# Kernel tuning notes

Measured on AMD Instinct MI355X. Metric: run time of the kernel, lower is better.

Reference implementation:

```python
import jax, jax.numpy as jnp
import numpy as np
import math

N, E, D, H = 1536, 49152, 512, 8
DH = D // H  # head dim = 64
SCALE = 256.0 * math.sqrt(2.0)  # rel_dists scaling in forward


def sinusoidal_pe(x, d):
    """x: [...] float positions -> [..., d] interleaved sin/cos encoding."""
    div = jnp.exp(jnp.arange(0, d, 2, dtype=jnp.float32) * (-math.log(10000.0) / d))
    ang = x[..., None] * div  # [..., d//2]
    return jnp.stack([jnp.sin(ang), jnp.cos(ang)], axis=-1).reshape(*x.shape, d)


def setup_inputs() -> dict:
    key = jax.random.key(0)
    ks = jax.random.split(key, 8)
    features = jax.random.normal(ks[0], (N, D), dtype=jnp.float32)
    edge_index = jax.random.randint(ks[1], (2, E), 0, N, dtype=jnp.int64)
    edge_attr = jax.random.uniform(ks[2], (E,), dtype=jnp.float32)  # normalized distances
    pos = jax.random.uniform(ks[3], (N, 2), dtype=jnp.float32)  # unused by forward
    s = 1.0 / math.sqrt(D)  # ~xavier-uniform bound sqrt(6/(D+D))... use simple symmetric init
    Wq = jax.random.uniform(ks[4], (D, D), minval=-s, maxval=s, dtype=jnp.float32)
    Wk = jax.random.uniform(ks[5], (D, D), minval=-s, maxval=s, dtype=jnp.float32)
    Wv = jax.random.uniform(ks[6], (D, D), minval=-s, maxval=s, dtype=jnp.float32)
    bq = jnp.zeros((D,), jnp.float32)
    bk = jnp.zeros((D,), jnp.float32)
    bv = jnp.zeros((D,), jnp.float32)
    return dict(features=features, edge_index=edge_index, edge_attr=edge_attr, pos=pos,
                Wq=Wq, bq=bq, Wk=Wk, bk=bk, Wv=Wv, bv=bv)


def reference(features, edge_index, edge_attr, pos, Wq, bq, Wk, bk, Wv, bv):
    # batch dim is 1 in the original (features.unsqueeze(0)); we omit it.
    q = (features @ Wq.T + bq).reshape(N, H, DH).transpose(1, 0, 2)  # [H,N,DH]
    k = (features @ Wk.T + bk).reshape(N, H, DH).transpose(1, 0, 2)
    v = (features @ Wv.T + bv).reshape(N, H, DH).transpose(1, 0, 2)

    qk = jnp.einsum('hqd,hrd->hqr', q, k)  # [H,N,N]

    # to_dense_adj: scatter-add edge_attr into dense [N,N], then scale
    rel = jnp.zeros((N, N), jnp.float32).at[edge_index[0], edge_index[1]].add(edge_attr) * SCALE
    # embed_k and embed_q are identical parameter-free sinusoidal encodings of rel
    rk = sinusoidal_pe(rel, DH)  # [N,N,DH]

    # original: qk + q.rk + k.rq + (q_repeat*k_repeat == qk)  => 2*qk + q.rk + k.rk
    logits = 2.0 * qk \
        + jnp.einsum('hqd,qrd->hqr', q, rk) \
        + jnp.einsum('hrd,qrd->hqr', k, rk)
    attn = jax.nn.softmax(logits / math.sqrt(DH), axis=-1)  # [H,N,N]

    out = jnp.einsum('hqr,hrd->hqd', attn, v)  # [H,N,DH]
    out = out.transpose(1, 0, 2).reshape(N, D)  # [N,D]
    return out.max(axis=0)  # [D] max-pool over nodes (MIL pooling)
```

## Files before the change

kernel.cpp:

```cpp
#include <hip/hip_runtime.h>
#include <cmath>


constexpr int Nn  = 1536;
constexpr int Dd  = 512;
constexpr int Hh  = 8;
constexpr int DHd = 64;
constexpr int SPLITS = 8;
constexpr float SCALE_F = 362.03867196751236f;
constexpr float M0 = 8.0f;

typedef float f4 __attribute__((ext_vector_type(4)));
typedef int   i4 __attribute__((ext_vector_type(4)));
typedef __attribute__((ext_vector_type(4))) float f32x4;
typedef __attribute__((ext_vector_type(8))) short bf16x8;

__device__ inline unsigned short bf16_rne(float x) {
    unsigned u = __float_as_uint(x);
    unsigned r = u + 0x7fff + ((u >> 16) & 1);
    return (unsigned short)(r >> 16);
}
__device__ inline float bf16_tof(unsigned short h) {
    return __uint_as_float(((unsigned)h) << 16);
}

__global__ __launch_bounds__(256) void pack_fw_k(
    const float* __restrict__ feat,
    const float* __restrict__ Wq, const float* __restrict__ Wk, const float* __restrict__ Wv,
    unsigned short* __restrict__ pFh, unsigned short* __restrict__ pFl,
    unsigned short* __restrict__ pWh, unsigned short* __restrict__ pWl)
{
    int tg = blockIdx.x * 256 + threadIdx.x;
    int type = blockIdx.y;
    int L = tg & 63;
    int kc = (tg >> 6) & 15;
    int t10 = tg >> 10;
    const float* src;
    unsigned short *oh, *ol;
    int row, col;
    if (type == 0) {
        src = feat; oh = pFh; ol = pFl;
        row = t10 * 16 + (L & 15);
        col = kc * 32 + (L >> 4) * 8;
    } else {
        int z = t10 >> 5, nt = t10 & 31;
        src = (z == 0) ? Wq : (z == 1) ? Wk : Wv;
        oh = pWh; ol = pWl;
        row = nt * 16 + (L & 15);
        col = kc * 32 + (L >> 4) * 8;
    }
    f4 a = *(const f4*)(src + (size_t)row * Dd + col);
    f4 b = *(const f4*)(src + (size_t)row * Dd + col + 4);
    float x[8];
    #pragma unroll
    for (int j = 0; j < 4; ++j) { x[j] = a[j]; x[4 + j] = b[j]; }
    unsigned short hs[8], ls[8];
    #pragma unroll
    for (int j = 0; j < 8; ++j) {
        hs[j] = bf16_rne(x[j]);
        ls[j] = bf16_rne(x[j] - bf16_tof(hs[j]));
    }
    *(bf16x8*)(oh + (size_t)tg * 8) = *(bf16x8*)hs;
    *(bf16x8*)(ol + (size_t)tg * 8) = *(bf16x8*)ls;
}

__global__ __launch_bounds__(256) void qkvm_k(
    const unsigned short* __restrict__ pFh, const unsigned short* __restrict__ pFl,
    const unsigned short* __restrict__ pWh, const unsigned short* __restrict__ pWl,
    const float* __restrict__ bq, const float* __restrict__ bk, const float* __restrict__ bv,
    float* __restrict__ Qo, float* __restrict__ Ko, float* __restrict__ Vo)
{
    const int lin = blockIdx.x + 8 * (blockIdx.y + 24 * blockIdx.z);
    const int swz = (lin & 7) * 72 + (lin >> 3);
    const int bx  = swz & 7;
    const int rem = swz >> 3;
    const int by  = rem % 24;
    const int bz  = rem / 24;

    const float* __restrict__ bias = (bz == 0) ? bq : (bz == 1) ? bk : bv;
    float* __restrict__ outp       = (bz == 0) ? Qo : (bz == 1) ? Ko : Vo;
    const int tid = threadIdx.x;
    const int L = tid & 63, wv = tid >> 6;
    const int l15 = L & 15, quad = L >> 4;
    const int mt0 = by * 4 + (wv & 1) * 2;
    const int nt0 = bx * 4 + (wv >> 1) * 2;

    f32x4 acc[2][2];
    #pragma unroll
    for (int i = 0; i < 2; ++i)
        #pragma unroll
        for (int j = 0; j < 2; ++j) acc[i][j] = (f32x4){0.f, 0.f, 0.f, 0.f};

    for (int kc = 0; kc < 16; ++kc) {
        bf16x8 ah[2], al[2], bh[2], bl[2];
        #pragma unroll
        for (int i = 0; i < 2; ++i) {
            size_t ao = ((size_t)((mt0 + i) * 16 + kc)) * 512 + L * 8;
            ah[i] = *(const bf16x8*)(pFh + ao);
            al[i] = *(const bf16x8*)(pFl + ao);
            size_t bo = ((size_t)((bz * 32 + nt0 + i) * 16 + kc)) * 512 + L * 8;
            bh[i] = *(const bf16x8*)(pWh + bo);
            bl[i] = *(const bf16x8*)(pWl + bo);
        }
        #pragma unroll
        for (int i = 0; i < 2; ++i)
            #pragma unroll
            for (int j = 0; j < 2; ++j) {
                f32x4 a = acc[i][j];
                a = __builtin_amdgcn_mfma_f32_16x16x32_bf16(ah[i], bh[j], a, 0, 0, 0);
                a = __builtin_amdgcn_mfma_f32_16x16x32_bf16(ah[i], bl[j], a, 0, 0, 0);
                a = __builtin_amdgcn_mfma_f32_16x16x32_bf16(al[i], bh[j], a, 0, 0, 0);
                a = __builtin_amdgcn_mfma_f32_16x16x32_bf16(al[i], bl[j], a, 0, 0, 0);
                acc[i][j] = a;
            }
    }

    #pragma unroll
    for (int i = 0; i < 2; ++i) {
        int row0 = (mt0 + i) * 16 + quad * 4;
        #pragma unroll
        for (int j = 0; j < 2; ++j) {
            int col = (nt0 + j) * 16 + l15;
            float b = bias[col];
            #pragma unroll
            for (int reg = 0; reg < 4; ++reg)
                outp[(size_t)(row0 + reg) * Dd + col] = acc[i][j][reg] + b;
        }
    }
}

__global__ __launch_bounds__(256) void pack_k(
    const float* __restrict__ Q, const float* __restrict__ K, const float* __restrict__ V,
    unsigned short* __restrict__ pQh, unsigned short* __restrict__ pQl,
    unsigned short* __restrict__ pKh, unsigned short* __restrict__ pKl,
    unsigned short* __restrict__ pVh, unsigned short* __restrict__ pVl)
{
    int tg = blockIdx.x * 256 + threadIdx.x;
    int type = blockIdx.y;
    int L = tg & 63;
    float x[8];
    unsigned short* oh;
    unsigned short* ol;
    if (type < 2) {
        const float* src = type ? K : Q;
        oh = type ? pKh : pQh;
        ol = type ? pKl : pQl;
        int kc = (tg >> 6) & 1;
        int mt = (tg >> 7) % 96;
        int h  = (tg >> 7) / 96;
        int row = mt * 16 + (L & 15);
        int col = h * 64 + kc * 32 + (L >> 4) * 8;
        f4 a = *(const f4*)(src + (size_t)row * Dd + col);
        f4 b = *(const f4*)(src + (size_t)row * Dd + col + 4);
        float sc = type ? 1.0f : 0.25f;
        #pragma unroll
        for (int j = 0; j < 4; ++j) { x[j] = a[j] * sc; x[4 + j] = b[j] * sc; }
    } else {
        oh = pVh; ol = pVl;
        int dt = (tg >> 6) & 3;
        int rc = (tg >> 8) % 48;
        int h  = (tg >> 8) / 48;
        int col  = h * 64 + dt * 16 + (L & 15);
        int row0 = rc * 32 + (L >> 4) * 8;
        #pragma unroll
        for (int j = 0; j < 8; ++j) x[j] = V[(size_t)(row0 + j) * Dd + col];
    }
    unsigned short hs[8], ls[8];
    #pragma unroll
    for (int j = 0; j < 8; ++j) {
        hs[j] = bf16_rne(x[j]);
        ls[j] = bf16_rne(x[j] - bf16_tof(hs[j]));
    }
    *(bf16x8*)(oh + (size_t)tg * 8) = *(bf16x8*)hs;
    *(bf16x8*)(ol + (size_t)tg * 8) = *(bf16x8*)ls;
}

__global__ __launch_bounds__(256) void init_rel_k(float* __restrict__ rel, int* __restrict__ eid)
{
    size_t i = ((size_t)blockIdx.x * 256 + threadIdx.x) * 4;
    if (i < (size_t)Nn * Nn) {
        *(f4*)(rel + i) = (f4){0.f, 0.f, 0.f, 0.f};
        *(i4*)(eid + i) = (i4){-1, -1, -1, -1};
    }
}

__global__ __launch_bounds__(256) void scatter_k(
    const int* __restrict__ raw, const float* __restrict__ attr,
    float* __restrict__ rel, int* __restrict__ eid, int* __restrict__ idxn, int E)
{
    int e = blockIdx.x * 256 + threadIdx.x;
    if (e >= E) return;
    int acc = 0;
    #pragma unroll
    for (int i = 0; i < 16; ++i) acc |= raw[2 * i + 1];
    int s, t;
    if (acc == 0) { s = raw[2 * e]; t = raw[2 * (E + e)]; }
    else          { s = raw[e];     t = raw[E + e]; }
    idxn[e] = s; idxn[E + e] = t;
    size_t off = (size_t)s * Nn + t;
    atomicAdd(rel + off, attr[e] * SCALE_F);
    eid[off] = e;
}

__global__ void oddsum_k(const float* __restrict__ Q, const float* __restrict__ K,
                         float* __restrict__ qodd, float* __restrict__ kodd,
                         float* __restrict__ koddT)
{
    int t = blockIdx.x * 256 + threadIdx.x;
    if (t >= 2 * Nn * Hh) return;
    const float* src = (t < Nn * Hh) ? Q : K;
    int i = (t < Nn * Hh) ? t : t - Nn * Hh;
    int n = i >> 3, h = i & 7;
    const float* row = src + (size_t)n * Dd + h * DHd;
    float s = 0.f;
    #pragma unroll
    for (int ii = 0; ii < 32; ++ii) s += row[2 * ii + 1];
    if (t < Nn * Hh) qodd[i] = s;
    else { kodd[i] = s; koddT[h * Nn + n] = 0.125f * s; }
}

__global__ __launch_bounds__(256) void delta_k(
    const int* __restrict__ idxn, const float* __restrict__ rel,
    const float* __restrict__ Q, const float* __restrict__ K,
    const float* __restrict__ qodd, const float* __restrict__ kodd,
    float* __restrict__ delta8, int E)
{
    int t = blockIdx.x * 256 + threadIdx.x;
    if (t >= E * Hh) return;
    int e = t >> 3, h = t & 7;
    int qi = idxn[e], ri = idxn[E + e];
    float x = rel[(size_t)qi * Nn + ri];
    const float* qrow = Q + (size_t)qi * Dd + h * DHd;
    const float* krow = K + (size_t)ri * Dd + h * DHd;
    float acc = 0.f;
    #pragma unroll
    for (int i = 0; i < 32; i += 2) {
        float d0 = expf(-0.28782313662425572f * (float)i);
        float d1 = expf(-0.28782313662425572f * (float)(i + 1));
        float s0, c0, s1, c1;
        __sincosf(x * d0, &s0, &c0);
        __sincosf(x * d1, &s1, &c1);
        f4 q4 = *(const f4*)(qrow + 2 * i);
        f4 k4 = *(const f4*)(krow + 2 * i);
        acc += (q4[0] + k4[0]) * s0 + (q4[1] + k4[1]) * c0
             + (q4[2] + k4[2]) * s1 + (q4[3] + k4[3]) * c1;
    }
    delta8[(size_t)e * Hh + h] = 0.125f * (acc - qodd[qi * Hh + h] - kodd[ri * Hh + h]);
}

__global__ __launch_bounds__(64, 3) void flash5_k(
    const unsigned short* __restrict__ pQh, const unsigned short* __restrict__ pQl,
    const unsigned short* __restrict__ pKh, const unsigned short* __restrict__ pKl,
    const unsigned short* __restrict__ pVh, const unsigned short* __restrict__ pVl,
    const int* __restrict__ eid, const float* __restrict__ delta8,
    const float* __restrict__ koddT,
    float* __restrict__ Opart, float* __restrict__ Lpart)
{
    const int lin = blockIdx.x + 96 * (blockIdx.y + 8 * blockIdx.z);
    const int swz = (lin & 7) * (96 * Hh * SPLITS / 8) + (lin >> 3);
    const int qt  = swz % 96;
    const int hs  = swz / 96;
    const int h   = hs & 7;
    const int s   = hs >> 3;

    const int L = threadIdx.x, quad = L >> 4, l15 = L & 15;
    const int q0 = qt * 16;
    __shared__ unsigned short phi[16][80];
    __shared__ unsigned short plo[16][80];

    bf16x8 qh[2], ql[2];
    #pragma unroll
    for (int kc = 0; kc < 2; ++kc) {
        size_t off = ((size_t)((h * 96 + qt) * 2 + kc)) * 512 + L * 8;
        qh[kc] = *(const bf16x8*)(pQh + off);
        ql[kc] = *(const bf16x8*)(pQl + off);
    }

    f32x4 O[4];
    float lsum[4];
    #pragma unroll
    for (int r = 0; r < 4; ++r) { lsum[r] = 0.f; O[r] = (f32x4){0.f, 0.f, 0.f, 0.f}; }

    const int NT = 24 / SPLITS;
    const int Tbase = s * NT;

    bf16x8 kh0[4], kh1[4], kl0[4], kl1[4];
    {
        const int r0 = Tbase * 64;
        #pragma unroll
        for (int nt = 0; nt < 4; ++nt) {
            size_t b0 = ((size_t)((h * 96 + (r0 >> 4) + nt) * 2)) * 512 + L * 8;
            kh0[nt] = *(const bf16x8*)(pKh + b0);
            kh1[nt] = *(const bf16x8*)(pKh + b0 + 512);
            kl0[nt] = *(const bf16x8*)(pKl + b0);
            kl1[nt] = *(const bf16x8*)(pKl + b0 + 512);
        }
    }

    float kvcur[4], dcur[16];
    {
        const int r0 = Tbase * 64;
        int ecur[16];
        #pragma unroll
        for (int nt = 0; nt < 4; ++nt) {
            kvcur[nt] = koddT[h * Nn + r0 + nt * 16 + l15];
            #pragma unroll
            for (int reg = 0; reg < 4; ++reg)
                ecur[nt * 4 + reg] = eid[(size_t)(q0 + quad * 4 + reg) * Nn + r0 + nt * 16 + l15];
        }
        #pragma unroll
        for (int i = 0; i < 16; ++i) {
            int e = ecur[i];
            float d = delta8[(size_t)(e < 0 ? 0 : e) * Hh + h];
            dcur[i] = (e >= 0) ? d : 0.f;
        }
    }

    for (int T = 0; T < NT; ++T) {
        const int r0 = (Tbase + T) * 64;
        const bool more = (T + 1 < NT);

        int   enxt[16];
        float kvnxt[4];
        if (more) {
            const int r1 = r0 + 64;
            #pragma unroll
            for (int nt = 0; nt < 4; ++nt) {
                kvnxt[nt] = koddT[h * Nn + r1 + nt * 16 + l15];
                #pragma unroll
                for (int reg = 0; reg < 4; ++reg)
                    enxt[nt * 4 + reg] = eid[(size_t)(q0 + quad * 4 + reg) * Nn + r1 + nt * 16 + l15];
            }
        }

        bf16x8 vh0[4], vh1[4], vl0[4], vl1[4];
        #pragma unroll
        for (int dt = 0; dt < 4; ++dt) {
            size_t vb = ((size_t)((h * 48 + (r0 >> 5)) * 4 + dt)) * 512 + L * 8;
            vh0[dt] = *(const bf16x8*)(pVh + vb);
            vh1[dt] = *(const bf16x8*)(pVh + vb + 2048);
            vl0[dt] = *(const bf16x8*)(pVl + vb);
            vl1[dt] = *(const bf16x8*)(pVl + vb + 2048);
        }

        f32x4 S[4];
        #pragma unroll
        for (int nt = 0; nt < 4; ++nt) {
            f32x4 a = {0.f, 0.f, 0.f, 0.f};
            a = __builtin_amdgcn_mfma_f32_16x16x32_bf16(qh[0], kh0[nt], a, 0, 0, 0);
            a = __builtin_amdgcn_mfma_f32_16x16x32_bf16(qh[1], kh1[nt], a, 0, 0, 0);
            a = __builtin_amdgcn_mfma_f32_16x16x32_bf16(qh[0], kl0[nt], a, 0, 0, 0);
            a = __builtin_amdgcn_mfma_f32_16x16x32_bf16(qh[1], kl1[nt], a, 0, 0, 0);
            a = __builtin_amdgcn_mfma_f32_16x16x32_bf16(ql[0], kh0[nt], a, 0, 0, 0);
            a = __builtin_amdgcn_mfma_f32_16x16x32_bf16(ql[1], kh1[nt], a, 0, 0, 0);
            S[nt] = a;
        }

        if (more) {
            const int r1 = r0 + 64;
            #pragma unroll
            for (int nt = 0; nt < 4; ++nt) {
                size_t b0 = ((size_t)((h * 96 + (r1 >> 4) + nt) * 2)) * 512 + L * 8;
                kh0[nt] = *(const bf16x8*)(pKh + b0);
                kh1[nt] = *(const bf16x8*)(pKh + b0 + 512);
                kl0[nt] = *(const bf16x8*)(pKl + b0);
                kl1[nt] = *(const bf16x8*)(pKl + b0 + 512);
            }
        }

        #pragma unroll
        for (int reg = 0; reg < 4; ++reg) {
            float p[4];
            #pragma unroll
            for (int nt = 0; nt < 4; ++nt) {
                p[nt] = __expf(S[nt][reg] + kvcur[nt] + dcur[nt * 4 + reg] - M0);
                lsum[reg] += p[nt];
                unsigned short hi = bf16_rne(p[nt]);
                phi[quad * 4 + reg][nt * 16 + l15] = hi;
                plo[quad * 4 + reg][nt * 16 + l15] = bf16_rne(p[nt] - bf16_tof(hi));
            }
        }

        bf16x8 ph[2], pl[2];
        #pragma unroll
        for (int kc2 = 0; kc2 < 2; ++kc2) {
            ph[kc2] = *(const bf16x8*)&phi[l15][kc2 * 32 + quad * 8];
            pl[kc2] = *(const bf16x8*)&plo[l15][kc2 * 32 + quad * 8];
        }

        #pragma unroll
        for (int dt = 0; dt < 4; ++dt) {
            f32x4 a = O[dt];
            a = __builtin_amdgcn_mfma_f32_16x16x32_bf16(ph[0], vh0[dt], a, 0, 0, 0);
            a = __builtin_amdgcn_mfma_f32_16x16x32_bf16(ph[1], vh1[dt], a, 0, 0, 0);
            a = __builtin_amdgcn_mfma_f32_16x16x32_bf16(ph[0], vl0[dt], a, 0, 0, 0);
            a = __builtin_amdgcn_mfma_f32_16x16x32_bf16(ph[1], vl1[dt], a, 0, 0, 0);
            a = __builtin_amdgcn_mfma_f32_16x16x32_bf16(pl[0], vh0[dt], a, 0, 0, 0);
            a = __builtin_amdgcn_mfma_f32_16x16x32_bf16(pl[1], vh1[dt], a, 0, 0, 0);
            O[dt] = a;
        }

        if (more) {
            #pragma unroll
            for (int i = 0; i < 16; ++i) {
                int e = enxt[i];
                float d = delta8[(size_t)(e < 0 ? 0 : e) * Hh + h];
                dcur[i] = (e >= 0) ? d : 0.f;
            }
            #pragma unroll
            for (int nt = 0; nt < 4; ++nt) kvcur[nt] = kvnxt[nt];
        }
    }

    #pragma unroll
    for (int reg = 0; reg < 4; ++reg) {
        #pragma unroll
        for (int o = 1; o < 16; o <<= 1) lsum[reg] += __shfl_xor(lsum[reg], o);
    }

    #pragma unroll
    for (int dt = 0; dt < 4; ++dt)
        #pragma unroll
        for (int reg = 0; reg < 4; ++reg)
            Opart[((size_t)(s * Hh + h) * Nn + q0 + quad * 4 + reg) * 64 + dt * 16 + l15] = O[dt][reg];
    if (l15 == 0) {
        #pragma unroll
        for (int reg = 0; reg < 4; ++reg)
            Lpart[(size_t)(s * Hh + h) * Nn + q0 + quad * 4 + reg] = lsum[reg];
    }
}

__global__ __launch_bounds__(256) void combine_mp_k(
    const float* __restrict__ Opart, const float* __restrict__ Lpart,
    float* __restrict__ partial)
{
    const int b = blockIdx.x;
    const int t = threadIdx.x;
    const int cg = (t & 127) * 4;
    const int h = cg >> 6, d = cg & 63;
    const int rh = t >> 7;
    f4 mx = {-3.0e38f, -3.0e38f, -3.0e38f, -3.0e38f};
    for (int r = 0; r < 8; ++r) {
        int q = b * 16 + rh * 8 + r;
        float l = 0.f;
        f4 o = {0.f, 0.f, 0.f, 0.f};
        #pragma unroll
        for (int s2 = 0; s2 < SPLITS; ++s2) {
            l += Lpart[(size_t)(s2 * Hh + h) * Nn + q];
            f4 ov = *(const f4*)(Opart + ((size_t)(s2 * Hh + h) * Nn + q) * 64 + d);
            #pragma unroll
            for (int c = 0; c < 4; ++c) o[c] += ov[c];
        }
        float inv = 1.0f / l;
        #pragma unroll
        for (int c = 0; c < 4; ++c) mx[c] = fmaxf(mx[c], o[c] * inv);
    }
    *(f4*)(partial + (size_t)(b * 2 + rh) * 512 + cg) = mx;
}

__global__ __launch_bounds__(128) void mp2_k(const float* __restrict__ partial,
                                             float* __restrict__ outp)
{
    const int t = threadIdx.x;
    f4 mx = {-3.0e38f, -3.0e38f, -3.0e38f, -3.0e38f};
    for (int b = 0; b < 192; ++b) {
        f4 v = *(const f4*)(partial + (size_t)b * 512 + 4 * t);
        #pragma unroll
        for (int c = 0; c < 4; ++c) mx[c] = fmaxf(mx[c], v[c]);
    }
    *(f4*)(outp + 4 * t) = mx;
}

extern "C" void kernel_launch(void* const* d_in, const int* in_sizes, int n_in,
                              void* d_out, int out_size, void* d_ws, size_t ws_size,
                              hipStream_t stream)
{
    const float* feat   = (const float*)d_in[0];
    const int*   rawidx = (const int*)d_in[1];
    const float* attr   = (const float*)d_in[2];
    const float* Wq = (const float*)d_in[4];
    const float* bq = (const float*)d_in[5];
    const float* Wk = (const float*)d_in[6];
    const float* bk = (const float*)d_in[7];
    const float* Wv = (const float*)d_in[8];
    const float* bv = (const float*)d_in[9];
    float* outp = (float*)d_out;
    const int E = in_sizes[2];

    const size_t ND_ = (size_t)Nn * Dd;
    const size_t NN_ = (size_t)Nn * Nn;
    const size_t PK_ = (size_t)Hh * 96 * 2 * 512;

    float* ws    = (float*)d_ws;
    float* Q     = ws;
    float* K     = Q + ND_;
    float* V     = K + ND_;
    float* rel   = V + ND_;
    unsigned short* pFh = (unsigned short*)(rel + NN_);
    unsigned short* pFl = pFh + PK_;
    unsigned short* pWh = pFl + PK_;
    unsigned short* pWl = pWh + PK_;
    int*   eid   = (int*)(pWl + PK_);
    float* delta8 = (float*)(eid + NN_);
    float* qodd  = delta8 + (size_t)E * Hh;
    float* kodd  = qodd + (size_t)Nn * Hh;
    float* koddT = kodd + (size_t)Nn * Hh;
    int*   idxn  = (int*)(koddT + (size_t)Nn * Hh);
    unsigned short* pQh = (unsigned short*)(idxn + 2 * E);
    unsigned short* pQl = pQh + PK_;
    unsigned short* pKh = pQl + PK_;
    unsigned short* pKl = pKh + PK_;
    unsigned short* pVh = pKl + PK_;
    unsigned short* pVl = pVh + PK_;
    float* Lpart = (float*)(pVl + PK_);
    float* partial = Lpart + (size_t)SPLITS * Hh * Nn;
    float* Opart = ws;

    pack_fw_k<<<dim3(384, 2), 256, 0, stream>>>(feat, Wq, Wk, Wv, pFh, pFl, pWh, pWl);
    qkvm_k<<<dim3(8, 24, 3), 256, 0, stream>>>(pFh, pFl, pWh, pWl, bq, bk, bv, Q, K, V);
    init_rel_k<<<(int)((NN_ / 4 + 255) / 256), 256, 0, stream>>>(rel, eid);
    scatter_k<<<(E + 255) / 256, 256, 0, stream>>>(rawidx, attr, rel, eid, idxn, E);
    oddsum_k<<<(2 * Nn * Hh + 255) / 256, 256, 0, stream>>>(Q, K, qodd, kodd, koddT);
    delta_k<<<(E * Hh + 255) / 256, 256, 0, stream>>>(idxn, rel, Q, K, qodd, kodd, delta8, E);
    pack_k<<<dim3(384, 3), 256, 0, stream>>>(Q, K, V, pQh, pQl, pKh, pKl, pVh, pVl);
    flash5_k<<<dim3(96, 8, SPLITS), 64, 0, stream>>>(pQh, pQl, pKh, pKl, pVh, pVl,
                                                     eid, delta8, koddT, Opart, Lpart);
    combine_mp_k<<<96, 256, 0, stream>>>(Opart, Lpart, partial);
    mp2_k<<<1, 128, 0, stream>>>(partial, outp);
}
```

Baseline: 201.7 us.

## Pack four query-tile waves per flash block and parallelize final max-pool reduction

The flash kernel now runs 4 independent 64-lane waves per 256-thread block, each handling its own 16-row query tile with per-wave LDS scratch, which cuts the block count by 4x. The combine kernel is spread over 384 blocks instead of 96, and the single-block final max reduction is split into a 32-block stage plus a small final stage. Masked delta loads become conditional instead of clamped. The aim is less launch and scheduling overhead and less serial tail work, at the cost of a changed occupancy profile and one extra kernel launch.

```diff
diff --git a/kernel.cpp b/kernel.cpp
--- a/kernel.cpp
+++ b/kernel.cpp
@@ -248,7 +248,7 @@
     delta8[(size_t)e * Hh + h] = 0.125f * (acc - qodd[qi * Hh + h] - kodd[ri * Hh + h]);
 }
 
-__global__ __launch_bounds__(64, 3) void flash5_k(
+__global__ __launch_bounds__(256, 4) void flash6_k(
     const unsigned short* __restrict__ pQh, const unsigned short* __restrict__ pQl,
     const unsigned short* __restrict__ pKh, const unsigned short* __restrict__ pKl,
     const unsigned short* __restrict__ pVh, const unsigned short* __restrict__ pVl,
@@ -256,17 +256,19 @@
     const float* __restrict__ koddT,
     float* __restrict__ Opart, float* __restrict__ Lpart)
 {
-    const int lin = blockIdx.x + 96 * (blockIdx.y + 8 * blockIdx.z);
-    const int swz = (lin & 7) * (96 * Hh * SPLITS / 8) + (lin >> 3);
-    const int qt  = swz % 96;
-    const int hs  = swz / 96;
+    const int lin = blockIdx.x + 24 * (blockIdx.y + 8 * blockIdx.z);
+    const int swz = (lin & 7) * 192 + (lin >> 3);
+    const int qtb = swz % 24;
+    const int hs  = swz / 24;
     const int h   = hs & 7;
     const int s   = hs >> 3;
 
-    const int L = threadIdx.x, quad = L >> 4, l15 = L & 15;
-    const int q0 = qt * 16;
-    __shared__ unsigned short phi[16][80];
-    __shared__ unsigned short plo[16][80];
+    const int w   = threadIdx.x >> 6;
+    const int qt  = qtb * 4 + w;
+    const int L   = threadIdx.x & 63, quad = L >> 4, l15 = L & 15;
+    const int q0  = qt * 16;
+    __shared__ unsigned short phi[4][16][80];
+    __shared__ unsigned short plo[4][16][80];
 
     bf16x8 qh[2], ql[2];
     #pragma unroll
@@ -311,8 +313,9 @@
         #pragma unroll
         for (int i = 0; i < 16; ++i) {
             int e = ecur[i];
-            float d = delta8[(size_t)(e < 0 ? 0 : e) * Hh + h];
-            dcur[i] = (e >= 0) ? d : 0.f;
+            float d = 0.f;
+            if (e >= 0) d = delta8[(size_t)e * Hh + h];
+            dcur[i] = d;
         }
     }
 
@@ -376,16 +379,16 @@
                 p[nt] = __expf(S[nt][reg] + kvcur[nt] + dcur[nt * 4 + reg] - M0);
                 lsum[reg] += p[nt];
                 unsigned short hi = bf16_rne(p[nt]);
-                phi[quad * 4 + reg][nt * 16 + l15] = hi;
-                plo[quad * 4 + reg][nt * 16 + l15] = bf16_rne(p[nt] - bf16_tof(hi));
+                phi[w][quad * 4 + reg][nt * 16 + l15] = hi;
+                plo[w][quad * 4 + reg][nt * 16 + l15] = bf16_rne(p[nt] - bf16_tof(hi));
             }
         }
 
         bf16x8 ph[2], pl[2];
         #pragma unroll
         for (int kc2 = 0; kc2 < 2; ++kc2) {
-            ph[kc2] = *(const bf16x8*)&phi[l15][kc2 * 32 + quad * 8];
-            pl[kc2] = *(const bf16x8*)&plo[l15][kc2 * 32 + quad * 8];
+            ph[kc2] = *(const bf16x8*)&phi[w][l15][kc2 * 32 + quad * 8];
+            pl[kc2] = *(const bf16x8*)&plo[w][l15][kc2 * 32 + quad * 8];
         }
 
         #pragma unroll
@@ -404,8 +407,9 @@
             #pragma unroll
             for (int i = 0; i < 16; ++i) {
                 int e = enxt[i];
-                float d = delta8[(size_t)(e < 0 ? 0 : e) * Hh + h];
-                dcur[i] = (e >= 0) ? d : 0.f;
+                float d = 0.f;
+                if (e >= 0) d = delta8[(size_t)e * Hh + h];
+                dcur[i] = d;
             }
             #pragma unroll
             for (int nt = 0; nt < 4; ++nt) kvcur[nt] = kvnxt[nt];
@@ -440,8 +444,8 @@
     const int h = cg >> 6, d = cg & 63;
     const int rh = t >> 7;
     f4 mx = {-3.0e38f, -3.0e38f, -3.0e38f, -3.0e38f};
-    for (int r = 0; r < 8; ++r) {
-        int q = b * 16 + rh * 8 + r;
+    for (int r = 0; r < 2; ++r) {
+        int q = b * 4 + rh * 2 + r;
         float l = 0.f;
         f4 o = {0.f, 0.f, 0.f, 0.f};
         #pragma unroll
@@ -458,13 +462,27 @@
     *(f4*)(partial + (size_t)(b * 2 + rh) * 512 + cg) = mx;
 }
 
-__global__ __launch_bounds__(128) void mp2_k(const float* __restrict__ partial,
-                                             float* __restrict__ outp)
-{
+__global__ __launch_bounds__(128) void mp2a_k(const float* __restrict__ partial,
+                                              float* __restrict__ partial2)
+{
+    const int b = blockIdx.x;
     const int t = threadIdx.x;
     f4 mx = {-3.0e38f, -3.0e38f, -3.0e38f, -3.0e38f};
-    for (int b = 0; b < 192; ++b) {
-        f4 v = *(const f4*)(partial + (size_t)b * 512 + 4 * t);
+    for (int i = 0; i < 24; ++i) {
+        f4 v = *(const f4*)(partial + (size_t)(b * 24 + i) * 512 + 4 * t);
+        #pragma unroll
+        for (int c = 0; c < 4; ++c) mx[c] = fmaxf(mx[c], v[c]);
+    }
+    *(f4*)(partial2 + (size_t)b * 512 + 4 * t) = mx;
+}
+
+__global__ __launch_bounds__(128) void mp2b_k(const float* __restrict__ partial2,
+                                              float* __restrict__ outp)
+{
+    const int t = threadIdx.x;
+    f4 mx = {-3.0e38f, -3.0e38f, -3.0e38f, -3.0e38f};
+    for (int b = 0; b < 32; ++b) {
+        f4 v = *(const f4*)(partial2 + (size_t)b * 512 + 4 * t);
         #pragma unroll
         for (int c = 0; c < 4; ++c) mx[c] = fmaxf(mx[c], v[c]);
     }
@@ -514,6 +532,7 @@
     unsigned short* pVl = pVh + PK_;
     float* Lpart = (float*)(pVl + PK_);
     float* partial = Lpart + (size_t)SPLITS * Hh * Nn;
+    float* partial2 = partial + (size_t)768 * 512;
     float* Opart = ws;
 
     pack_fw_k<<<dim3(384, 2), 256, 0, stream>>>(feat, Wq, Wk, Wv, pFh, pFl, pWh, pWl);
@@ -523,8 +542,9 @@
     oddsum_k<<<(2 * Nn * Hh + 255) / 256, 256, 0, stream>>>(Q, K, qodd, kodd, koddT);
     delta_k<<<(E * Hh + 255) / 256, 256, 0, stream>>>(idxn, rel, Q, K, qodd, kodd, delta8, E);
     pack_k<<<dim3(384, 3), 256, 0, stream>>>(Q, K, V, pQh, pQl, pKh, pKl, pVh, pVl);
-    flash5_k<<<dim3(96, 8, SPLITS), 64, 0, stream>>>(pQh, pQl, pKh, pKl, pVh, pVl,
-                                                     eid, delta8, koddT, Opart, Lpart);
-    combine_mp_k<<<96, 256, 0, stream>>>(Opart, Lpart, partial);
-    mp2_k<<<1, 128, 0, stream>>>(partial, outp);
-}
+    flash6_k<<<dim3(24, 8, SPLITS), 256, 0, stream>>>(pQh, pQl, pKh, pKl, pVh, pVl,
+                                                      eid, delta8, koddT, Opart, Lpart);
+    combine_mp_k<<<384, 256, 0, stream>>>(Opart, Lpart, partial);
+    mp2a_k<<<32, 128, 0, stream>>>(partial, partial2);
+    mp2b_k<<<1, 128, 0, stream>>>(partial2, outp);
+}
```

Result: slower. 232.7 us (+15.3%).
